# Kernel optimization log

Hardware: AMD Instinct MI355X
Metric: run time of the kernel (lower is better)

Reference implementation:

```python
import jax, jax.numpy as jnp
import numpy as np

NPOINT = 512
RADIUS = 0.2
NSAMPLE = 32
EPS = 1e-5  # BatchNorm eps


def _fps(x, npoint):
    """Farthest point sampling. x: [B,N,3] -> idx [B,npoint] int32.
    Deterministic start at index 0 (original uses a random start index)."""
    B, N, _ = x.shape

    def step(carry, _):
        dist, far = carry
        c = jnp.take_along_axis(x, far[:, None, None], axis=1)  # [B,1,3]
        d = jnp.sum((x - c) ** 2, axis=-1)                      # [B,N]
        dist = jnp.minimum(dist, d)
        return (dist, jnp.argmax(dist, axis=-1).astype(jnp.int32)), far

    init = (jnp.full((B, N), 1e10, x.dtype), jnp.zeros((B,), jnp.int32))
    _, cent = jax.lax.scan(step, init, None, length=npoint)  # [npoint,B]
    return cent.T


def _gather(pts, idx):
    # pts: [B,N,C], idx: [B,...] -> [B,...,C]
    return jax.vmap(lambda a, i: a[i])(pts, idx)


def _sqdist(a, b):
    # a: [B,S,3], b: [B,N,3] -> [B,S,N]  (same expansion as square_distance)
    return (jnp.sum(a ** 2, -1, keepdims=True)
            + jnp.sum(b ** 2, -1)[:, None, :]
            - 2.0 * jnp.einsum('bsc,bnc->bsn', a, b))


def _bn_relu(h, g, be):
    # training-mode BatchNorm over (B,S,K), channel-last h: [B,S,K,C]
    m = jnp.mean(h, axis=(0, 1, 2))
    v = jnp.var(h, axis=(0, 1, 2))
    return jax.nn.relu((h - m) * jax.lax.rsqrt(v + EPS) * g + be)


def _forward(xyz, points, params):
    x = jnp.transpose(xyz, (0, 2, 1))     # [B,N,3]
    p = jnp.transpose(points, (0, 2, 1))  # [B,N,D]
    B, N, _ = x.shape

    fps_idx = _fps(x, NPOINT)             # [B,S]
    new_xyz = _gather(x, fps_idx)         # [B,S,3]

    # ball query: keep indices within radius, sort, take first NSAMPLE,
    # pad misses with the first valid index (same as torch code)
    sqr = _sqdist(new_xyz, x)             # [B,S,N]
    gi = jnp.where(sqr <= RADIUS * RADIUS, jnp.arange(N)[None, None, :], N)
    gi = jnp.sort(gi, axis=-1)[:, :, :NSAMPLE]  # [B,S,K]
    gi = jnp.where(gi == N, gi[:, :, :1], gi)

    grouped_xyz = _gather(x, gi) - new_xyz[:, :, None, :]  # [B,S,K,3]
    grouped_p = _gather(p, gi)                             # [B,S,K,D]
    h = jnp.concatenate([grouped_xyz, grouped_p], axis=-1)  # [B,S,K,3+D]

    for (W, b, g, be) in params:  # shared 1x1 conv == per-point linear
        h = _bn_relu(jnp.einsum('bskc,oc->bsko', h, W) + b, g, be)

    new_points = jnp.transpose(jnp.max(h, axis=2), (0, 2, 1))  # [B,C_out,S]
    return jnp.transpose(new_xyz, (0, 2, 1)), new_points       # [B,3,S], [B,C,S]


def setup_inputs() -> dict:
    key = jax.random.key(0)
    ks = jax.random.split(key, 10)
    B, N, D = 16, 4096, 3
    inp = {
        'xyz': jax.random.uniform(ks[0], (B, 3, N), jnp.float32),
        'points': jax.random.uniform(ks[1], (B, D, N), jnp.float32),
    }
    dims = [(6, 64), (64, 64), (64, 128)]
    for i, (cin, cout) in enumerate(dims):
        inp[f'W{i}'] = jax.random.normal(ks[2 + 2 * i], (cout, cin), jnp.float32) * 0.1
        inp[f'b{i}'] = jax.random.normal(ks[3 + 2 * i], (cout,), jnp.float32) * 0.1
        inp[f'g{i}'] = jnp.ones((cout,), jnp.float32)
        inp[f'be{i}'] = jnp.zeros((cout,), jnp.float32)
    return inp


def reference(xyz, points, W0, b0, g0, be0, W1, b1, g1, be1, W2, b2, g2, be2):
    params = [(W0, b0, g0, be0), (W1, b1, g1, be1), (W2, b2, g2, be2)]
    return _forward(xyz, points, params)
```

## Files before the change

### kernel.cpp

```cpp
#include <hip/hip_runtime.h>
#include <hip/hip_bf16.h>

#define BB 16
#define NN 4096
#define SS 512
#define KK 32
#define CNTF 262144.0f
#define FT 256
#define FP 16

typedef short bf16x8 __attribute__((ext_vector_type(8)));
typedef float f32x4 __attribute__((ext_vector_type(4)));

__device__ __forceinline__ unsigned short f2bf(float x) {
  __hip_bfloat16 h = __float2bfloat16(x);
  return *reinterpret_cast<unsigned short*>(&h);
}

#define DPP_COMBINE(kk, CTRL)                                                         \
  {                                                                                   \
    unsigned lo_ = (unsigned)(kk), hi_ = (unsigned)((kk) >> 32);                      \
    unsigned plo_ = (unsigned)__builtin_amdgcn_update_dpp(0, (int)lo_, (CTRL), 0xF, 0xF, true); \
    unsigned phi_ = (unsigned)__builtin_amdgcn_update_dpp(0, (int)hi_, (CTRL), 0xF, 0xF, true); \
    unsigned long long ok_ = ((unsigned long long)phi_ << 32) | plo_;                 \
    kk = (kk) > ok_ ? (kk) : ok_;                                                     \
  }

__global__ __launch_bounds__(FT) void k_fps(const float* __restrict__ xyz,
                                            float* __restrict__ newxyz,
                                            float* __restrict__ dout) {
  __shared__ __align__(16) float4 ps[NN];
  __shared__ __align__(16) unsigned long long sKey[2][4];
  const int b = blockIdx.x;
  const int tid = threadIdx.x;
  const int wid = tid >> 6;
  const float* px = xyz + (size_t)b * 3 * NN;
  float lx[FP], ly[FP], lz[FP], dist[FP];
#pragma unroll
  for (int j = 0; j < FP; j++) {
    int n = j * FT + tid;
    float x = px[n], y = px[NN + n], z = px[2 * NN + n];
    lx[j] = x; ly[j] = y; lz[j] = z;
    ps[n] = make_float4(x, y, z, 0.f);
    dist[j] = 1e10f;
  }
  __syncthreads();
  float cx = px[0], cy = px[NN], cz = px[2 * NN];
  float c0x = 0.f, c0y = 0.f, c0z = 0.f, c1x = 0.f, c1y = 0.f, c1z = 0.f;
  for (int s = 0;; s++) {
    bool cap = (tid == (s & 255));
    if (s < 256) {
      if (cap) { c0x = cx; c0y = cy; c0z = cz; }
    } else {
      if (cap) { c1x = cx; c1y = cy; c1z = cz; }
    }
    if (s == SS - 1) break;
    float bestd = -1.0f;
    unsigned bestn = 0u;
#pragma unroll
    for (int j = 0; j < FP; j++) {
      float dx = __fsub_rn(lx[j], cx);
      float dy = __fsub_rn(ly[j], cy);
      float dz = __fsub_rn(lz[j], cz);
      float d = __fadd_rn(__fadd_rn(__fmul_rn(dx, dx), __fmul_rn(dy, dy)), __fmul_rn(dz, dz));
      float dm = fminf(dist[j], d);
      dist[j] = dm;
      if (dm > bestd) { bestd = dm; bestn = (unsigned)(j * FT + tid); }
    }
    unsigned long long wbest =
        ((unsigned long long)__float_as_uint(bestd) << 32) | (unsigned)(~bestn);
    DPP_COMBINE(wbest, 0xB1);
    DPP_COMBINE(wbest, 0x4E);
    DPP_COMBINE(wbest, 0x141);
    DPP_COMBINE(wbest, 0x140);
    DPP_COMBINE(wbest, 0x142);
    DPP_COMBINE(wbest, 0x143);
    int p = s & 1;
    if ((tid & 63) == 63) sKey[p][wid] = wbest;
    __syncthreads();
    const ulonglong2* kp = (const ulonglong2*)&sKey[p][0];
    ulonglong2 v0 = kp[0], v1 = kp[1];
    unsigned long long ka = (v0.y > v0.x) ? v0.y : v0.x;
    unsigned long long kb = (v1.y > v1.x) ? v1.y : v1.x;
    unsigned long long km = (kb > ka) ? kb : ka;
    unsigned n = ~(unsigned)km;
    float4 c4 = ps[n];
    cx = c4.x; cy = c4.y; cz = c4.z;
  }
  {
    float* nx0 = newxyz + ((size_t)b * SS + tid) * 3;
    nx0[0] = c0x; nx0[1] = c0y; nx0[2] = c0z;
    float* nx1 = newxyz + ((size_t)b * SS + 256 + tid) * 3;
    nx1[0] = c1x; nx1[1] = c1y; nx1[2] = c1z;
    float* d0 = dout + (size_t)b * 3 * SS;
    d0[tid] = c0x;        d0[SS + tid] = c0y;        d0[2 * SS + tid] = c0z;
    d0[256 + tid] = c1x;  d0[SS + 256 + tid] = c1y;  d0[2 * SS + 256 + tid] = c1z;
  }
}

__global__ __launch_bounds__(256) void k_ball(const float* __restrict__ xyz,
                                              const float* __restrict__ newxyz,
                                              int* __restrict__ gi) {
  const int lane = threadIdx.x & 63;
  const int w = threadIdx.x >> 6;
  const int idx = blockIdx.x * 4 + w;
  const int b = idx >> 9;
  const float* px = xyz + (size_t)b * 3 * NN;
  const float* c = newxyz + (size_t)idx * 3;
  const double R2 = 0.2 * 0.2;
  double cx = (double)c[0], cy = (double)c[1], cz = (double)c[2];
  double ca = cx * cx + cy * cy + cz * cz;
  int total = 0;
  int first_n = 0;
  bool found = false;
  unsigned long long lt = (1ull << lane) - 1ull;
  for (int chunk = 0; chunk < NN / 64; chunk++) {
    int n = chunk * 64 + lane;
    double x = (double)px[n], y = (double)px[NN + n], z = (double)px[2 * NN + n];
    double sb = x * x + y * y + z * z;
    double dot = cx * x + cy * y + cz * z;
    double sqr = (ca + sb) - 2.0 * dot;
    bool in = sqr <= R2;
    unsigned long long m = __ballot(in);
    if (!found && m) { first_n = chunk * 64 + __builtin_ctzll(m); found = true; }
    int rank = total + __popcll(m & lt);
    if (in && rank < KK) gi[(size_t)idx * KK + rank] = n;
    total += __popcll(m);
    if (total >= KK) break;
  }
  if (total < KK) {
    for (int slot = total + lane; slot < KK; slot += 64) gi[(size_t)idx * KK + slot] = first_n;
  }
}

__global__ __launch_bounds__(256) void k_group(const float* __restrict__ xyz,
                                               const float* __restrict__ pts,
                                               const float* __restrict__ newxyz,
                                               const int* __restrict__ gi,
                                               float* __restrict__ h0) {
  int m = blockIdx.x * 256 + threadIdx.x;
  int b = m >> 14;
  int bs = m >> 5;
  int n = gi[m];
  const float* px = xyz + (size_t)b * 3 * NN;
  const float* pp = pts + (size_t)b * 3 * NN;
  const float* c = newxyz + (size_t)bs * 3;
  float* o = h0 + (size_t)m * 6;
  o[0] = px[n] - c[0];
  o[1] = px[NN + n] - c[1];
  o[2] = px[2 * NN + n] - c[2];
  o[3] = pp[n];
  o[4] = pp[NN + n];
  o[5] = pp[2 * NN + n];
}

__global__ __launch_bounds__(256) void k_l1stats(const float* __restrict__ h0,
                                                 const float* __restrict__ W0,
                                                 const float* __restrict__ b0,
                                                 float* __restrict__ part) {
  __shared__ float hs[256 * 6];
  __shared__ float sred[512];
  int tid = threadIdx.x;
  int base = blockIdx.x * 256;
  for (int t = tid; t < 1536; t += 256) hs[t] = h0[(size_t)base * 6 + t];
  __syncthreads();
  int c = tid & 63, g = tid >> 6;
  float w[6];
#pragma unroll
  for (int j = 0; j < 6; j++) w[j] = W0[c * 6 + j];
  float bb = b0[c];
  float s1 = 0.f, s2 = 0.f;
  for (int i = g; i < 256; i += 4) {
    float v = bb;
#pragma unroll
    for (int j = 0; j < 6; j++) v = fmaf(w[j], hs[i * 6 + j], v);
    s1 += v; s2 = fmaf(v, v, s2);
  }
  sred[tid] = s1; sred[256 + tid] = s2;
  __syncthreads();
  if (tid < 64) {
    float a = 0.f, q = 0.f;
#pragma unroll
    for (int g2 = 0; g2 < 4; g2++) { a += sred[tid + 64 * g2]; q += sred[256 + tid + 64 * g2]; }
    part[blockIdx.x * 256 + tid] = a;
    part[blockIdx.x * 256 + 128 + tid] = q;
  }
}

__global__ __launch_bounds__(256) void k_reduce(const float* __restrict__ part, int NBLK,
                                                const float* __restrict__ gamma,
                                                const float* __restrict__ beta,
                                                float* __restrict__ scale,
                                                float* __restrict__ shift) {
  __shared__ float sr[512];
  int c = blockIdx.x;
  int tid = threadIdx.x;
  float s1 = 0.f, s2 = 0.f;
  for (int nb = tid; nb < NBLK; nb += 256) {
    s1 += part[(size_t)nb * 256 + c];
    s2 += part[(size_t)nb * 256 + 128 + c];
  }
  sr[tid] = s1; sr[256 + tid] = s2;
  __syncthreads();
  for (int off = 128; off >= 1; off >>= 1) {
    if (tid < off) { sr[tid] += sr[tid + off]; sr[256 + tid] += sr[256 + tid + off]; }
    __syncthreads();
  }
  if (tid == 0) {
    float m = sr[0] / CNTF;
    float v = sr[256] / CNTF - m * m;
    float sc = gamma[c] / sqrtf(v + 1e-5f);
    scale[c] = sc;
    shift[c] = beta[c] - m * sc;
  }
}

__global__ __launch_bounds__(256) void k_l2(const float* __restrict__ h0,
                                            const float* __restrict__ W0,
                                            const float* __restrict__ b0,
                                            const float* __restrict__ scale1,
                                            const float* __restrict__ shift1,
                                            const float* __restrict__ W1,
                                            const float* __restrict__ b1,
                                            __hip_bfloat16* __restrict__ l2,
                                            float* __restrict__ part) {
  __shared__ float hs[128 * 6];
  __shared__ __align__(16) float a1s[128 * 64];
  __shared__ float sred[512];
  int tid = threadIdx.x;
  int base = blockIdx.x * 128;
  for (int t = tid; t < 768; t += 256) hs[t] = h0[(size_t)base * 6 + t];
  __syncthreads();
  for (int t = tid; t < 8192; t += 256) {
    int i = t >> 6, c = t & 63;
    float v = b0[c];
#pragma unroll
    for (int j = 0; j < 6; j++) v = fmaf(W0[c * 6 + j], hs[i * 6 + j], v);
    a1s[t] = fmaxf(fmaf(scale1[c], v, shift1[c]), 0.f);
  }
  __syncthreads();
  int c = tid & 63, g = tid >> 6;
  float w[64];
#pragma unroll
  for (int j = 0; j < 64; j++) w[j] = W1[c * 64 + j];
  float bb = b1[c];
  float s1 = 0.f, s2 = 0.f;
  for (int i = g; i < 128; i += 4) {
    float acc = bb;
    const float4* ap = (const float4*)(a1s + i * 64);
#pragma unroll
    for (int j4 = 0; j4 < 16; j4++) {
      float4 a = ap[j4];
      acc = fmaf(w[4 * j4 + 0], a.x, acc);
      acc = fmaf(w[4 * j4 + 1], a.y, acc);
      acc = fmaf(w[4 * j4 + 2], a.z, acc);
      acc = fmaf(w[4 * j4 + 3], a.w, acc);
    }
    l2[(size_t)(base + i) * 64 + c] = __float2bfloat16(acc);
    s1 += acc; s2 = fmaf(acc, acc, s2);
  }
  sred[tid] = s1; sred[256 + tid] = s2;
  __syncthreads();
  if (tid < 64) {
    float a = 0.f, q = 0.f;
#pragma unroll
    for (int g2 = 0; g2 < 4; g2++) { a += sred[tid + 64 * g2]; q += sred[256 + tid + 64 * g2]; }
    part[blockIdx.x * 256 + tid] = a;
    part[blockIdx.x * 256 + 128 + tid] = q;
  }
}

__global__ __launch_bounds__(256) void k_l3pass(const __hip_bfloat16* __restrict__ l2,
                                                const float* __restrict__ scale2,
                                                const float* __restrict__ shift2,
                                                const float* __restrict__ W2,
                                                const float* __restrict__ b2,
                                                float* __restrict__ part,
                                                float* __restrict__ pmax) {
  __shared__ __align__(16) unsigned short a2s[128][64];
  __shared__ __align__(16) unsigned short w2s[128][64];
  __shared__ float sst1[128][17];
  __shared__ float sst2[128][17];
  __shared__ float smx[128][17];
  __shared__ float sb2[128];
  int tid = threadIdx.x;
  size_t base = (size_t)blockIdx.x * 128;
  for (int t = tid; t < 8192; t += 256) {
    int i = t >> 6, k = t & 63;
    float v = __bfloat162float(l2[base * 64 + t]);
    float a = fmaxf(fmaf(scale2[k], v, shift2[k]), 0.f);
    int kc = (k >> 3) ^ (i & 7);
    a2s[i][kc * 8 + (k & 7)] = f2bf(a);
  }
  for (int t = tid; t < 8192; t += 256) {
    int n = t >> 6, k = t & 63;
    int kc = (k >> 3) ^ (n & 7);
    w2s[n][kc * 8 + (k & 7)] = f2bf(W2[t]);
  }
  if (tid < 128) sb2[tid] = b2[tid];
  __syncthreads();
  int w = tid >> 6, l = tid & 63, lr = l & 15, lk = l >> 4;
  bf16x8 A[2][2];
#pragma unroll
  for (int mt = 0; mt < 2; mt++) {
    int row = (w * 2 + mt) * 16 + lr;
#pragma unroll
    for (int kb = 0; kb < 2; kb++) {
      int kc = (kb * 4 + lk) ^ (row & 7);
      A[mt][kb] = *(const bf16x8*)&a2s[row][kc * 8];
    }
  }
  f32x4 acc[2][8];
#pragma unroll
  for (int mt = 0; mt < 2; mt++)
#pragma unroll
    for (int nt = 0; nt < 8; nt++) acc[mt][nt] = f32x4{0.f, 0.f, 0.f, 0.f};
#pragma unroll
  for (int nt = 0; nt < 8; nt++) {
    int n = nt * 16 + lr;
    int kc0 = lk ^ (n & 7);
    int kc1 = (4 + lk) ^ (n & 7);
    bf16x8 B0 = *(const bf16x8*)&w2s[n][kc0 * 8];
    bf16x8 B1 = *(const bf16x8*)&w2s[n][kc1 * 8];
#pragma unroll
    for (int mt = 0; mt < 2; mt++) {
      acc[mt][nt] = __builtin_amdgcn_mfma_f32_16x16x32_bf16(A[mt][0], B0, acc[mt][nt], 0, 0, 0);
      acc[mt][nt] = __builtin_amdgcn_mfma_f32_16x16x32_bf16(A[mt][1], B1, acc[mt][nt], 0, 0, 0);
    }
  }
  int slot = w * 4 + lk;
#pragma unroll
  for (int nt = 0; nt < 8; nt++) {
    int c = nt * 16 + lr;
    float bias = sb2[c];
    float s1 = 0.f, s2 = 0.f, mx = -3.4e38f;
#pragma unroll
    for (int mt = 0; mt < 2; mt++)
#pragma unroll
      for (int r = 0; r < 4; r++) {
        float v = acc[mt][nt][r] + bias;
        s1 += v; s2 = fmaf(v, v, s2); mx = fmaxf(mx, v);
      }
    sst1[c][slot] = s1; sst2[c][slot] = s2; smx[c][slot] = mx;
  }
  __syncthreads();
  if (tid < 128) {
    int c = tid;
    float s1 = 0.f, s2 = 0.f;
#pragma unroll
    for (int t = 0; t < 16; t++) { s1 += sst1[c][t]; s2 += sst2[c][t]; }
    part[blockIdx.x * 256 + c] = s1;
    part[blockIdx.x * 256 + 128 + c] = s2;
#pragma unroll
    for (int q = 0; q < 4; q++) {
      float m = fmaxf(fmaxf(smx[c][4 * q + 0], smx[c][4 * q + 1]),
                      fmaxf(smx[c][4 * q + 2], smx[c][4 * q + 3]));
      pmax[((size_t)blockIdx.x * 4 + q) * 128 + c] = m;
    }
  }
}

__global__ __launch_bounds__(256) void k_bn3(const float* __restrict__ pmax,
                                             const float* __restrict__ scale3,
                                             const float* __restrict__ shift3,
                                             float* __restrict__ dout) {
  __shared__ float tile[32][129];
  int tid = threadIdx.x;
  int b = blockIdx.x >> 4;
  int s0 = (blockIdx.x & 15) * 32;
  const float* src = pmax + ((size_t)b * SS + s0) * 128;
  for (int t = tid; t < 4096; t += 256) {
    int r = t >> 7, c = t & 127;
    tile[r][c] = src[r * 128 + c];
  }
  __syncthreads();
  float* dst = dout + 24576 + (size_t)b * 128 * SS;
  for (int t = tid; t < 4096; t += 256) {
    int c = t >> 5, r = t & 31;
    float v = tile[r][c];
    dst[(size_t)c * SS + s0 + r] = fmaxf(fmaf(scale3[c], v, shift3[c]), 0.f);
  }
}

extern "C" void kernel_launch(void* const* d_in, const int* in_sizes, int n_in,
                              void* d_out, int out_size, void* d_ws, size_t ws_size,
                              hipStream_t stream) {
  const float* xyz = (const float*)d_in[0];
  const float* pts = (const float*)d_in[1];
  const float* W0 = (const float*)d_in[2];
  const float* b0 = (const float*)d_in[3];
  const float* g0 = (const float*)d_in[4];
  const float* be0 = (const float*)d_in[5];
  const float* W1 = (const float*)d_in[6];
  const float* b1 = (const float*)d_in[7];
  const float* g1 = (const float*)d_in[8];
  const float* be1 = (const float*)d_in[9];
  const float* W2 = (const float*)d_in[10];
  const float* b2 = (const float*)d_in[11];
  const float* g2 = (const float*)d_in[12];
  const float* be2 = (const float*)d_in[13];
  float* out = (float*)d_out;

  char* ws = (char*)d_ws;
  int* gi = (int*)(ws + 32768);
  float* newxyz = (float*)(ws + 1081344);
  float* h0 = (float*)(ws + 1179648);
  float* pmax = h0;
  float* part = (float*)(ws + 7471104);
  float* scale1 = (float*)(ws + 9568256);
  float* shift1 = scale1 + 128;
  float* scale2 = shift1 + 128;
  float* shift2 = scale2 + 128;
  float* scale3 = shift2 + 128;
  float* shift3 = scale3 + 128;
  __hip_bfloat16* l2 = (__hip_bfloat16*)(ws + 9571328);

  k_fps<<<BB, FT, 0, stream>>>(xyz, newxyz, out);
  k_ball<<<2048, 256, 0, stream>>>(xyz, newxyz, gi);
  k_group<<<1024, 256, 0, stream>>>(xyz, pts, newxyz, gi, h0);
  k_l1stats<<<1024, 256, 0, stream>>>(h0, W0, b0, part);
  k_reduce<<<64, 256, 0, stream>>>(part, 1024, g0, be0, scale1, shift1);
  k_l2<<<2048, 256, 0, stream>>>(h0, W0, b0, scale1, shift1, W1, b1, l2, part);
  k_reduce<<<64, 256, 0, stream>>>(part, 2048, g1, be1, scale2, shift2);
  k_l3pass<<<2048, 256, 0, stream>>>(l2, scale2, shift2, W2, b2, part, pmax);
  k_reduce<<<128, 256, 0, stream>>>(part, 2048, g2, be2, scale3, shift3);
  k_bn3<<<256, 256, 0, stream>>>(pmax, scale3, shift3, out);
}
```

Before: 457.3 us.

## Fuse grouping with layer-1 stats and move layer-2 matmul to bf16 MFMA

Merges the grouping kernel with the layer-1 statistics kernel, so the gathered features go straight from registers into shared memory instead of being written to and re-read from the h0 buffer for the stats pass. Rewrites the layer-2 64x64 pointwise matmul from scalar FP32 FMAs over a 64-register weight array to bf16 MFMA 16x16x32, using XOR-swizzled shared-memory tiles for activations and weights. Statistics are reduced from per-lane MFMA accumulators through padded shared arrays. This trades FP32 precision in the layer-2 inputs for bf16, which can shift the BatchNorm statistics slightly.

Result: faster. 426.9 us (median of 3 runs) (-6.6%).

```diff
diff --git a/kernel.cpp b/kernel.cpp
--- a/kernel.cpp
+++ b/kernel.cpp
@@ -133,42 +133,41 @@
   }
 }
 
-__global__ __launch_bounds__(256) void k_group(const float* __restrict__ xyz,
-                                               const float* __restrict__ pts,
-                                               const float* __restrict__ newxyz,
-                                               const int* __restrict__ gi,
-                                               float* __restrict__ h0) {
-  int m = blockIdx.x * 256 + threadIdx.x;
+__global__ __launch_bounds__(256) void k_group_stats(const float* __restrict__ xyz,
+                                                     const float* __restrict__ pts,
+                                                     const float* __restrict__ newxyz,
+                                                     const int* __restrict__ gi,
+                                                     const float* __restrict__ W0,
+                                                     const float* __restrict__ b0,
+                                                     float* __restrict__ h0,
+                                                     float* __restrict__ part) {
+  __shared__ float hs[256 * 6];
+  __shared__ float sred[512];
+  int tid = threadIdx.x;
+  int base = blockIdx.x * 256;
+  int m = base + tid;
   int b = m >> 14;
   int bs = m >> 5;
   int n = gi[m];
   const float* px = xyz + (size_t)b * 3 * NN;
   const float* pp = pts + (size_t)b * 3 * NN;
   const float* c = newxyz + (size_t)bs * 3;
+  float f0 = px[n] - c[0];
+  float f1 = px[NN + n] - c[1];
+  float f2 = px[2 * NN + n] - c[2];
+  float f3 = pp[n];
+  float f4 = pp[NN + n];
+  float f5 = pp[2 * NN + n];
   float* o = h0 + (size_t)m * 6;
-  o[0] = px[n] - c[0];
-  o[1] = px[NN + n] - c[1];
-  o[2] = px[2 * NN + n] - c[2];
-  o[3] = pp[n];
-  o[4] = pp[NN + n];
-  o[5] = pp[2 * NN + n];
-}
-
-__global__ __launch_bounds__(256) void k_l1stats(const float* __restrict__ h0,
-                                                 const float* __restrict__ W0,
-                                                 const float* __restrict__ b0,
-                                                 float* __restrict__ part) {
-  __shared__ float hs[256 * 6];
-  __shared__ float sred[512];
-  int tid = threadIdx.x;
-  int base = blockIdx.x * 256;
-  for (int t = tid; t < 1536; t += 256) hs[t] = h0[(size_t)base * 6 + t];
-  __syncthreads();
-  int c = tid & 63, g = tid >> 6;
+  o[0] = f0; o[1] = f1; o[2] = f2; o[3] = f3; o[4] = f4; o[5] = f5;
+  float* hr = hs + tid * 6;
+  hr[0] = f0; hr[1] = f1; hr[2] = f2; hr[3] = f3; hr[4] = f4; hr[5] = f5;
+  __syncthreads();
+  int cc = tid & 63, g = tid >> 6;
   float w[6];
 #pragma unroll
-  for (int j = 0; j < 6; j++) w[j] = W0[c * 6 + j];
-  float bb = b0[c];
+  for (int j = 0; j < 6; j++) w[j] = W0[cc * 6 + j];
+  float bb = b0[cc];
   float s1 = 0.f, s2 = 0.f;
   for (int i = g; i < 256; i += 4) {
     float v = bb;
@@ -225,48 +224,84 @@
                                             __hip_bfloat16* __restrict__ l2,
                                             float* __restrict__ part) {
   __shared__ float hs[128 * 6];
-  __shared__ __align__(16) float a1s[128 * 64];
-  __shared__ float sred[512];
+  __shared__ __align__(16) unsigned short a1s[128][64];
+  __shared__ __align__(16) unsigned short w1s[64][64];
+  __shared__ float sst1[64][17];
+  __shared__ float sst2[64][17];
+  __shared__ float sb1[64];
   int tid = threadIdx.x;
   int base = blockIdx.x * 128;
   for (int t = tid; t < 768; t += 256) hs[t] = h0[(size_t)base * 6 + t];
+  for (int t = tid; t < 4096; t += 256) {
+    int n = t >> 6, k = t & 63;
+    int kc = (k >> 3) ^ (n & 7);
+    w1s[n][kc * 8 + (k & 7)] = f2bf(W1[t]);
+  }
+  if (tid < 64) sb1[tid] = b1[tid];
   __syncthreads();
   for (int t = tid; t < 8192; t += 256) {
-    int i = t >> 6, c = t & 63;
-    float v = b0[c];
-#pragma unroll
-    for (int j = 0; j < 6; j++) v = fmaf(W0[c * 6 + j], hs[i * 6 + j], v);
-    a1s[t] = fmaxf(fmaf(scale1[c], v, shift1[c]), 0.f);
-  }
-  __syncthreads();
-  int c = tid & 63, g = tid >> 6;
-  float w[64];
-#pragma unroll
-  for (int j = 0; j < 64; j++) w[j] = W1[c * 64 + j];
-  float bb = b1[c];
-  float s1 = 0.f, s2 = 0.f;
-  for (int i = g; i < 128; i += 4) {
-    float acc = bb;
-    const float4* ap = (const float4*)(a1s + i * 64);
-#pragma unroll
-    for (int j4 = 0; j4 < 16; j4++) {
-      float4 a = ap[j4];
-      acc = fmaf(w[4 * j4 + 0], a.x, acc);
-      acc = fmaf(w[4 * j4 + 1], a.y, acc);
-      acc = fmaf(w[4 * j4 + 2], a.z, acc);
-      acc = fmaf(w[4 * j4 + 3], a.w, acc);
-    }
-    l2[(size_t)(base + i) * 64 + c] = __float2bfloat16(acc);
-    s1 += acc; s2 = fmaf(acc, acc, s2);
-  }
-  sred[tid] = s1; sred[256 + tid] = s2;
+    int i = t >> 6, k = t & 63;
+    float v = b0[k];
+#pragma unroll
+    for (int j = 0; j < 6; j++) v = fmaf(W0[k * 6 + j], hs[i * 6 + j], v);
+    float a = fmaxf(fmaf(scale1[k], v, shift1[k]), 0.f);
+    int kc = (k >> 3) ^ (i & 7);
+    a1s[i][kc * 8 + (k & 7)] = f2bf(a);
+  }
+  __syncthreads();
+  int w = tid >> 6, l = tid & 63, lr = l & 15, lk = l >> 4;
+  bf16x8 A[2][2];
+#pragma unroll
+  for (int mt = 0; mt < 2; mt++) {
+    int row = (w * 2 + mt) * 16 + lr;
+#pragma unroll
+    for (int kb = 0; kb < 2; kb++) {
+      int kc = (kb * 4 + lk) ^ (row & 7);
+      A[mt][kb] = *(const bf16x8*)&a1s[row][kc * 8];
+    }
+  }
+  f32x4 acc[2][4];
+#pragma unroll
+  for (int mt = 0; mt < 2; mt++)
+#pragma unroll
+    for (int nt = 0; nt < 4; nt++) acc[mt][nt] = f32x4{0.f, 0.f, 0.f, 0.f};
+#pragma unroll
+  for (int nt = 0; nt < 4; nt++) {
+    int n = nt * 16 + lr;
+    int kc0 = lk ^ (n & 7);
+    int kc1 = (4 + lk) ^ (n & 7);
+    bf16x8 B0 = *(const bf16x8*)&w1s[n][kc0 * 8];
+    bf16x8 B1 = *(const bf16x8*)&w1s[n][kc1 * 8];
+#pragma unroll
+    for (int mt = 0; mt < 2; mt++) {
+      acc[mt][nt] = __builtin_amdgcn_mfma_f32_16x16x32_bf16(A[mt][0], B0, acc[mt][nt], 0, 0, 0);
+      acc[mt][nt] = __builtin_amdgcn_mfma_f32_16x16x32_bf16(A[mt][1], B1, acc[mt][nt], 0, 0, 0);
+    }
+  }
+  int slot = w * 4 + lk;
+#pragma unroll
+  for (int nt = 0; nt < 4; nt++) {
+    int cch = nt * 16 + lr;
+    float bias = sb1[cch];
+    float s1 = 0.f, s2 = 0.f;
+#pragma unroll
+    for (int mt = 0; mt < 2; mt++)
+#pragma unroll
+      for (int r = 0; r < 4; r++) {
+        float v = acc[mt][nt][r] + bias;
+        int row = (w * 2 + mt) * 16 + lk * 4 + r;
+        l2[(size_t)(base + row) * 64 + cch] = __float2bfloat16(v);
+        s1 += v; s2 = fmaf(v, v, s2);
+      }
+    sst1[cch][slot] = s1; sst2[cch][slot] = s2;
+  }
   __syncthreads();
   if (tid < 64) {
-    float a = 0.f, q = 0.f;
-#pragma unroll
-    for (int g2 = 0; g2 < 4; g2++) { a += sred[tid + 64 * g2]; q += sred[256 + tid + 64 * g2]; }
-    part[blockIdx.x * 256 + tid] = a;
-    part[blockIdx.x * 256 + 128 + tid] = q;
+    float s1 = 0.f, s2 = 0.f;
+#pragma unroll
+    for (int t = 0; t < 16; t++) { s1 += sst1[tid][t]; s2 += sst2[tid][t]; }
+    part[blockIdx.x * 256 + tid] = s1;
+    part[blockIdx.x * 256 + 128 + tid] = s2;
   }
 }
 
@@ -417,8 +452,7 @@
 
   k_fps<<<BB, FT, 0, stream>>>(xyz, newxyz, out);
   k_ball<<<2048, 256, 0, stream>>>(xyz, newxyz, gi);
-  k_group<<<1024, 256, 0, stream>>>(xyz, pts, newxyz, gi, h0);
-  k_l1stats<<<1024, 256, 0, stream>>>(h0, W0, b0, part);
+  k_group_stats<<<1024, 256, 0, stream>>>(xyz, pts, newxyz, gi, W0, b0, h0, part);
   k_reduce<<<64, 256, 0, stream>>>(part, 1024, g0, be0, scale1, shift1);
   k_l2<<<2048, 256, 0, stream>>>(h0, W0, b0, scale1, shift1, W1, b1, l2, part);
   k_reduce<<<64, 256, 0, stream>>>(part, 2048, g1, be1, scale2, shift2);
```
